# Performance work log

Measured on AMD Instinct MI355X. Metric: run time of the kernel, lower is better.

Reference implementation:

```python
import jax, jax.numpy as jnp
import numpy as np

LN_EPS = 1e-5


def setup_inputs() -> dict:
    key = jax.random.key(0)
    ks = jax.random.split(key, 4)
    B, L, Dm, N = 16, 2048, 512, 64
    return {
        "x": jax.random.normal(ks[0], (B, L, Dm), dtype=jnp.float32),
        "A": jax.random.normal(ks[1], (Dm, N), dtype=jnp.float32),
        "C": jax.random.normal(ks[2], (Dm, N), dtype=jnp.float32),
        "D": jax.random.normal(ks[3], (Dm,), dtype=jnp.float32),
        "gamma": jnp.ones((Dm,), dtype=jnp.float32),
        "beta": jnp.zeros((Dm,), dtype=jnp.float32),
    }


def reference(x, A, C, D, gamma, beta):
    # LayerNorm over last dim (matches nn.LayerNorm(d_model))
    mean = jnp.mean(x, axis=-1, keepdims=True)
    var = jnp.mean(jnp.square(x - mean), axis=-1, keepdims=True)
    x_norm = (x - mean) * jax.lax.rsqrt(var + LN_EPS) * gamma + beta

    B, L, Dm = x.shape
    N = A.shape[1]
    h0 = jnp.zeros((B, N), dtype=x.dtype)

    def step(h, u):
        # u: [B, Dm]; h: [B, N]
        h = jnp.tanh(u @ A + h)
        y = h @ C.T + u * D  # [B, Dm]
        return h, y

    # scan over time: xs [L, B, Dm]
    _, ys = jax.lax.scan(step, h0, jnp.swapaxes(x_norm, 0, 1))
    out = jnp.swapaxes(ys, 0, 1)  # [B, L, Dm]
    return out + x
```

## Files before the change

### kernel.cpp

```cpp
#include <hip/hip_runtime.h>
#include <hip/hip_bf16.h>

typedef short bf16x8 __attribute__((ext_vector_type(8)));
typedef float f32x4 __attribute__((ext_vector_type(4)));

constexpr int B_ = 16;
constexpr int L_ = 2048;
constexpr int DM = 512;
constexpr int NS = 64;
constexpr int BL = B_ * L_;
constexpr float LN_EPS = 1e-5f;
constexpr float KLN = 2.8853900817779268f;

constexpr int SEGS = 32;
constexpr int LSEG = L_ / SEGS;
constexpr int WARM = 64;

__device__ __forceinline__ unsigned f32bits(float f) {
    union { float f; unsigned u; } v{f}; return v.u;
}
__device__ __forceinline__ float bitsf32(unsigned u) {
    union { unsigned u; float f; } v{u}; return v.f;
}
__device__ __forceinline__ unsigned short f2bf(float f) {
    unsigned u = f32bits(f);
    unsigned r = u + 0x7FFF + ((u >> 16) & 1);
    return (unsigned short)(r >> 16);
}

__device__ __forceinline__ void norm_split8(float4 u0, float4 u1,
                                            float rstd, float m2,
                                            bf16x8& ah, bf16x8& al) {
    float t[8] = { fmaf(u0.x, rstd, m2), fmaf(u0.y, rstd, m2),
                   fmaf(u0.z, rstd, m2), fmaf(u0.w, rstd, m2),
                   fmaf(u1.x, rstd, m2), fmaf(u1.y, rstd, m2),
                   fmaf(u1.z, rstd, m2), fmaf(u1.w, rstd, m2) };
    unsigned hb[8], lb[8];
    #pragma unroll
    for (int j = 0; j < 8; ++j) {
        unsigned tb = f32bits(t[j]);
        hb[j] = tb & 0xFFFF0000u;
        lb[j] = f32bits(t[j] - bitsf32(hb[j]));
    }
    union { unsigned u[4]; bf16x8 v; } H, L;
    #pragma unroll
    for (int p = 0; p < 4; ++p) {
        H.u[p] = (hb[2*p] >> 16) | hb[2*p+1];
        L.u[p] = (lb[2*p] >> 16) | (lb[2*p+1] & 0xFFFF0000u);
    }
    ah = H.v; al = L.v;
}

__global__ __launch_bounds__(256) void k_pack(const float* __restrict__ A,
                                              const float* __restrict__ C,
                                              const float* __restrict__ gamma,
                                              const float* __restrict__ beta,
                                              const float* __restrict__ Dv,
                                              unsigned short* __restrict__ PAh,
                                              unsigned short* __restrict__ PAl,
                                              unsigned short* __restrict__ PC,
                                              float* __restrict__ c0,
                                              float* __restrict__ gd,
                                              float* __restrict__ bd) {
    const int blk = blockIdx.x;
    const int tid = threadIdx.x;
    if (blk < 32) {
        const int g = blk * 256 + tid;
        if (g < 4096) {
            const int lane = g & 63, ct = (g >> 6) & 3, k32 = (g >> 8) & 3, kc = g >> 10;
            const int kbase = kc * 128 + k32 * 32 + (lane >> 4) * 8;
            const int col   = ct * 16 + (lane & 15);
            unsigned hb[8], lb[8];
            #pragma unroll
            for (int j = 0; j < 8; ++j) {
                float v = gamma[kbase + j] * A[(size_t)(kbase + j) * NS + col];
                unsigned tb = f32bits(v);
                hb[j] = tb & 0xFFFF0000u;
                lb[j] = f32bits(v - bitsf32(hb[j]));
            }
            uint4 ph, pl;
            ph.x = (hb[0] >> 16) | hb[1]; ph.y = (hb[2] >> 16) | hb[3];
            ph.z = (hb[4] >> 16) | hb[5]; ph.w = (hb[6] >> 16) | hb[7];
            pl.x = (lb[0] >> 16) | (lb[1] & 0xFFFF0000u);
            pl.y = (lb[2] >> 16) | (lb[3] & 0xFFFF0000u);
            pl.z = (lb[4] >> 16) | (lb[5] & 0xFFFF0000u);
            pl.w = (lb[6] >> 16) | (lb[7] & 0xFFFF0000u);
            *reinterpret_cast<uint4*>(PAh + (size_t)g * 8) = ph;
            *reinterpret_cast<uint4*>(PAl + (size_t)g * 8) = pl;
        } else {
            const int g2 = g - 4096;
            const int d = g2 >> 3, s = g2 & 7;
            const int nbase = (s ^ (d & 7)) * 8;
            unsigned short v[8];
            #pragma unroll
            for (int j = 0; j < 8; ++j) v[j] = f2bf(C[(size_t)d * NS + nbase + j]);
            uint4 p;
            p.x = v[0] | ((unsigned)v[1] << 16); p.y = v[2] | ((unsigned)v[3] << 16);
            p.z = v[4] | ((unsigned)v[5] << 16); p.w = v[6] | ((unsigned)v[7] << 16);
            *reinterpret_cast<uint4*>(PC + (size_t)g2 * 8) = p;
        }
    } else {
        __shared__ float red[256];
        #pragma unroll
        for (int i = 0; i < 2; ++i) {
            int d = tid + 256 * i;
            gd[d] = gamma[d] * Dv[d];
            bd[d] = beta[d] * Dv[d];
        }
        const int n = tid & 63, part = tid >> 6;
        float s = 0.f;
        #pragma unroll 8
        for (int k = part * 128; k < part * 128 + 128; ++k)
            s += beta[k] * A[(size_t)k * NS + n];
        red[tid] = s;
        __syncthreads();
        if (tid < 64)
            c0[tid] = red[tid] + red[tid + 64] + red[tid + 128] + red[tid + 192];
    }
}

__global__ __launch_bounds__(512, 2) void k_gemmA(const float* __restrict__ x,
                                               const unsigned short* __restrict__ PAh,
                                               const unsigned short* __restrict__ PAl,
                                               const float* __restrict__ c0,
                                               float* __restrict__ stats,
                                               float* __restrict__ Bu) {
    __shared__ unsigned short AsH[4 * 16 * 64 * 8];
    __shared__ unsigned short AsL[4 * 16 * 64 * 8];
    const int tid  = threadIdx.x;
    const int r0   = blockIdx.x * 128;
    const int w    = tid >> 6;
    const int lane = tid & 63;
    const int myrow = 16 * w + (lane & 15);
    const int kb    = (lane >> 4) * 8;
    const float* xrow = x + (size_t)(r0 + myrow) * DM;

    {
        const float4* sh = reinterpret_cast<const float4*>(PAh);
        const float4* sl = reinterpret_cast<const float4*>(PAl);
        float4* dh = reinterpret_cast<float4*>(AsH);
        float4* dl = reinterpret_cast<float4*>(AsL);
        #pragma unroll
        for (int i = 0; i < 8; ++i) {
            dh[tid + 512 * i] = sh[tid + 512 * i];
            dl[tid + 512 * i] = sl[tid + 512 * i];
        }
    }

    float4 xv[32];
    #pragma unroll
    for (int kc = 0; kc < 4; ++kc) {
        #pragma unroll
        for (int k32 = 0; k32 < 4; ++k32) {
            xv[kc * 8 + 2 * k32]     = *reinterpret_cast<const float4*>(
                xrow + kc * 128 + k32 * 32 + kb);
            xv[kc * 8 + 2 * k32 + 1] = *reinterpret_cast<const float4*>(
                xrow + kc * 128 + k32 * 32 + kb + 4);
        }
    }

    float s = 0.f, s2 = 0.f;
    #pragma unroll
    for (int i = 0; i < 32; ++i) {
        float4 a = xv[i];
        s  += (a.x + a.y) + (a.z + a.w);
        s2 += a.x*a.x + a.y*a.y + a.z*a.z + a.w*a.w;
    }
    s += __shfl_xor(s, 16); s2 += __shfl_xor(s2, 16);
    s += __shfl_xor(s, 32); s2 += __shfl_xor(s2, 32);
    const float mean = s * (1.0f / DM);
    const float var  = s2 * (1.0f / DM) - mean * mean;
    const float rstd = rsqrtf(var + LN_EPS);
    const float m2   = -mean * rstd;
    if (lane < 16) {
        stats[2 * (r0 + myrow)]     = mean;
        stats[2 * (r0 + myrow) + 1] = rstd;
    }

    __syncthreads();

    f32x4 acc[4] = {};
    const bf16x8* ABh = reinterpret_cast<const bf16x8*>(AsH);
    const bf16x8* ABl = reinterpret_cast<const bf16x8*>(AsL);

    #pragma unroll
    for (int kc = 0; kc < 4; ++kc) {
        #pragma unroll
        for (int k32 = 0; k32 < 4; ++k32) {
            bf16x8 ah, al;
            norm_split8(xv[kc * 8 + 2 * k32], xv[kc * 8 + 2 * k32 + 1], rstd, m2, ah, al);
            #pragma unroll
            for (int ct = 0; ct < 4; ++ct) {
                const int fi = ((kc * 4 + k32) * 4 + ct) * 64 + lane;
                bf16x8 bh = ABh[fi];
                bf16x8 bl = ABl[fi];
                acc[ct] = __builtin_amdgcn_mfma_f32_16x16x32_bf16(ah, bh, acc[ct], 0, 0, 0);
                acc[ct] = __builtin_amdgcn_mfma_f32_16x16x32_bf16(ah, bl, acc[ct], 0, 0, 0);
                acc[ct] = __builtin_amdgcn_mfma_f32_16x16x32_bf16(al, bh, acc[ct], 0, 0, 0);
            }
        }
    }

    const int orow = r0 + 16 * w + (lane >> 4) * 4;
    #pragma unroll
    for (int ct = 0; ct < 4; ++ct) {
        const int n = ct * 16 + (lane & 15);
        const float c0n = c0[n];
        #pragma unroll
        for (int j = 0; j < 4; ++j)
            Bu[(size_t)(orow + j) * NS + n] = acc[ct][j] + c0n;
    }
}

__global__ __launch_bounds__(64) void k_scan(const float* __restrict__ Bu,
                                             unsigned short* __restrict__ h) {
    constexpr int G = 16;
    const int seg = blockIdx.x & (SEGS - 1);
    const int b   = blockIdx.x / SEGS;
    const int n   = threadIdx.x;
    const int l0     = seg * LSEG;
    const int start  = (seg == 0) ? 0 : (l0 - WARM);
    const int nGrp   = (l0 + LSEG - start) / G;
    const int gStore = (l0 - start) / G;

    const float* bp = Bu + (size_t)b * L_ * NS + n;
    unsigned short* hp = h + (size_t)b * L_ * NS + n;

    float bufA[G], bufB[G];
    #pragma unroll
    for (int j = 0; j < G; ++j) bufA[j] = KLN * bp[(size_t)(start + j) * NS];

    float hv = 0.0f;
    int g = 0;
    for (;;) {
        {
            const int base = start + (g + 1) * G;
            if (g + 1 < nGrp) {
                #pragma unroll
                for (int j = 0; j < G; ++j)
                    bufB[j] = KLN * bp[(size_t)(base + j) * NS];
            }
            unsigned short* hq = hp + (size_t)(start + g * G) * NS;
            const bool doStore = g >= gStore;
            #pragma unroll
            for (int j = 0; j < G; ++j) {
                float t = fmaf(hv, KLN, bufA[j]);
                float e = __builtin_amdgcn_exp2f(t);
                float rr = __builtin_amdgcn_rcpf(e + 1.0f);
                hv = fmaf(-2.0f, rr, 1.0f);
                if (doStore) hq[(size_t)j * NS] = f2bf(hv);
            }
        }
        if (++g == nGrp) break;
        {
            const int base = start + (g + 1) * G;
            if (g + 1 < nGrp) {
                #pragma unroll
                for (int j = 0; j < G; ++j)
                    bufA[j] = KLN * bp[(size_t)(base + j) * NS];
            }
            unsigned short* hq = hp + (size_t)(start + g * G) * NS;
            const bool doStore = g >= gStore;
            #pragma unroll
            for (int j = 0; j < G; ++j) {
                float t = fmaf(hv, KLN, bufB[j]);
                float e = __builtin_amdgcn_exp2f(t);
                float rr = __builtin_amdgcn_rcpf(e + 1.0f);
                hv = fmaf(-2.0f, rr, 1.0f);
                if (doStore) hq[(size_t)j * NS] = f2bf(hv);
            }
        }
        if (++g == nGrp) break;
    }
}

__global__ __launch_bounds__(256) void k_gemmC(const float* __restrict__ x,
                                               const unsigned short* __restrict__ PC,
                                               const float* __restrict__ gd,
                                               const float* __restrict__ bd,
                                               const float* __restrict__ stats,
                                               const unsigned short* __restrict__ h,
                                               float* __restrict__ out) {
    __shared__ unsigned short Hs[64 * 64];
    __shared__ unsigned short Cs[128 * 64];
    const int tid  = threadIdx.x;
    const int r0   = (blockIdx.x >> 2) * 64;
    const int d0   = (blockIdx.x & 3) * 128;
    const int w    = tid >> 6;
    const int lane = tid & 63;

    {
        const float4* src = reinterpret_cast<const float4*>(PC + (size_t)d0 * NS);
        float4* dst = reinterpret_cast<float4*>(Cs);
        #pragma unroll
        for (int i = 0; i < 4; ++i) dst[tid + 256 * i] = src[tid + 256 * i];
    }
    {
        const char* hb = reinterpret_cast<const char*>(h + (size_t)r0 * NS);
        #pragma unroll
        for (int it = 0; it < 2; ++it) {
            const int o   = it * 4096 + tid * 16;
            const int row = o >> 7;
            const int s   = (o >> 4) & 7;
            uint4 v = *reinterpret_cast<const uint4*>(hb + row * 128 + ((s ^ (row & 7)) << 4));
            *reinterpret_cast<uint4*>(reinterpret_cast<char*>(Hs) + o) = v;
        }
    }
    __syncthreads();

    f32x4 acc[8] = {};
    const int arow = 16 * w + (lane & 15);
    #pragma unroll
    for (int kt = 0; kt < 2; ++kt) {
        const int c = kt * 4 + (lane >> 4);
        bf16x8 a = *reinterpret_cast<const bf16x8*>(
            reinterpret_cast<char*>(Hs) + arow * 128 + ((c ^ (arow & 7)) << 4));
        #pragma unroll
        for (int ct = 0; ct < 8; ++ct) {
            const int dl = ct * 16 + (lane & 15);
            bf16x8 bfr = *reinterpret_cast<const bf16x8*>(
                reinterpret_cast<char*>(Cs) + dl * 128 + ((c ^ (dl & 7)) << 4));
            acc[ct] = __builtin_amdgcn_mfma_f32_16x16x32_bf16(a, bfr, acc[ct], 0, 0, 0);
        }
    }

    const int rbase = r0 + 16 * w + (lane >> 4) * 4;
    float mean_[4], rstd_[4];
    #pragma unroll
    for (int j = 0; j < 4; ++j) {
        mean_[j] = stats[2 * (rbase + j)];
        rstd_[j] = stats[2 * (rbase + j) + 1];
    }
    #pragma unroll
    for (int ct = 0; ct < 8; ++ct) {
        const int d  = d0 + ct * 16 + (lane & 15);
        const float gdv = gd[d];
        const float bdv = bd[d];
        #pragma unroll
        for (int j = 0; j < 4; ++j) {
            const size_t idx = (size_t)(rbase + j) * DM + d;
            const float xv = x[idx];
            const float z  = (xv - mean_[j]) * rstd_[j];
            out[idx] = acc[ct][j] + z * gdv + bdv + xv;
        }
    }
}

extern "C" void kernel_launch(void* const* d_in, const int* in_sizes, int n_in,
                              void* d_out, int out_size, void* d_ws, size_t ws_size,
                              hipStream_t stream) {
    const float* x     = (const float*)d_in[0];
    const float* A     = (const float*)d_in[1];
    const float* C     = (const float*)d_in[2];
    const float* Dv    = (const float*)d_in[3];
    const float* gamma = (const float*)d_in[4];
    const float* beta  = (const float*)d_in[5];
    float* out = (float*)d_out;

    char* ws = (char*)d_ws;
    float* Bu           = (float*)(ws);
    unsigned short* h   = (unsigned short*)(ws + (size_t)BL * NS * 4);
    float* stats        = (float*)(ws + (size_t)BL * NS * 6);
    char* p = ws + (size_t)BL * NS * 6 + (size_t)BL * 2 * 4;
    unsigned short* PAh = (unsigned short*)p;            p += (size_t)DM * NS * 2;
    unsigned short* PAl = (unsigned short*)p;            p += (size_t)DM * NS * 2;
    unsigned short* PC  = (unsigned short*)p;            p += (size_t)DM * NS * 2;
    float* c0           = (float*)p;                     p += 256;
    float* gd           = (float*)p;                     p += (size_t)DM * 4;
    float* bd           = (float*)p;

    k_pack<<<33, 256, 0, stream>>>(A, C, gamma, beta, Dv, PAh, PAl, PC, c0, gd, bd);
    k_gemmA<<<BL / 128, 512, 0, stream>>>(x, PAh, PAl, c0, stats, Bu);
    k_scan<<<B_ * SEGS, 64, 0, stream>>>(Bu, h);
    k_gemmC<<<(BL / 64) * (DM / 128), 256, 0, stream>>>(x, PC, gd, bd, stats, h, out);
}
```

Before: 73.75 us.

## Fuse scan with output GEMM, keeping hidden states in shared memory

Merges the segmented tanh scan and the C-projection GEMM into one kernel. Inside each 512-thread block, one wave runs the scan and writes bf16 hidden states into swizzled LDS, then all waves do the MFMA projection plus the LayerNorm skip epilogue. This removes the global round trip of h and one kernel launch. The cost is that 7 of 8 waves idle during the serial scan, and the C fragments are now read straight from global memory, unswizzled, instead of being staged in LDS.

```diff
diff --git a/kernel.cpp b/kernel.cpp
--- a/kernel.cpp
+++ b/kernel.cpp
@@ -89,11 +89,9 @@
             *reinterpret_cast<uint4*>(PAl + (size_t)g * 8) = pl;
         } else {
             const int g2 = g - 4096;
-            const int d = g2 >> 3, s = g2 & 7;
-            const int nbase = (s ^ (d & 7)) * 8;
             unsigned short v[8];
             #pragma unroll
-            for (int j = 0; j < 8; ++j) v[j] = f2bf(C[(size_t)d * NS + nbase + j]);
+            for (int j = 0; j < 8; ++j) v[j] = f2bf(C[(size_t)g2 * 8 + j]);
             uint4 p;
             p.x = v[0] | ((unsigned)v[1] << 16); p.y = v[2] | ((unsigned)v[3] << 16);
             p.z = v[4] | ((unsigned)v[5] << 16); p.w = v[6] | ((unsigned)v[7] << 16);
@@ -212,136 +210,125 @@
     }
 }
 
-__global__ __launch_bounds__(64) void k_scan(const float* __restrict__ Bu,
-                                             unsigned short* __restrict__ h) {
-    constexpr int G = 16;
+__global__ __launch_bounds__(512, 4) void k_scanC(const float* __restrict__ x,
+                                                  const unsigned short* __restrict__ PC,
+                                                  const float* __restrict__ gd,
+                                                  const float* __restrict__ bd,
+                                                  const float* __restrict__ stats,
+                                                  const float* __restrict__ Bu,
+                                                  float* __restrict__ out) {
+    __shared__ unsigned short Hs[64 * 64];
+    const int tid = threadIdx.x;
     const int seg = blockIdx.x & (SEGS - 1);
-    const int b   = blockIdx.x / SEGS;
-    const int n   = threadIdx.x;
-    const int l0     = seg * LSEG;
-    const int start  = (seg == 0) ? 0 : (l0 - WARM);
-    const int nGrp   = (l0 + LSEG - start) / G;
-    const int gStore = (l0 - start) / G;
-
-    const float* bp = Bu + (size_t)b * L_ * NS + n;
-    unsigned short* hp = h + (size_t)b * L_ * NS + n;
-
-    float bufA[G], bufB[G];
-    #pragma unroll
-    for (int j = 0; j < G; ++j) bufA[j] = KLN * bp[(size_t)(start + j) * NS];
-
-    float hv = 0.0f;
-    int g = 0;
-    for (;;) {
-        {
-            const int base = start + (g + 1) * G;
-            if (g + 1 < nGrp) {
+    const int b   = blockIdx.x >> 5;
+    const int l0  = seg * LSEG;
+    const int rowbase = b * L_ + l0;
+
+    if (tid < 64) {
+        constexpr int G = 16;
+        const int n     = tid;
+        const int start = (seg == 0) ? 0 : (l0 - WARM);
+        const int skip  = l0 - start;
+        const int nGrp  = (l0 + LSEG - start) / G;
+        const float* bp = Bu + ((size_t)b * L_ + start) * NS + n;
+        char* hbase = reinterpret_cast<char*>(Hs);
+
+        float bufA[G], bufB[G];
+        #pragma unroll
+        for (int j = 0; j < G; ++j) bufA[j] = KLN * bp[(size_t)j * NS];
+        float hv = 0.0f;
+        int g = 0;
+        for (;;) {
+            {
+                if (g + 1 < nGrp) {
+                    const int base = (g + 1) * G;
+                    #pragma unroll
+                    for (int j = 0; j < G; ++j)
+                        bufB[j] = KLN * bp[(size_t)(base + j) * NS];
+                }
+                const int lbase = g * G - skip;
+                const bool doStore = lbase >= 0;
                 #pragma unroll
-                for (int j = 0; j < G; ++j)
-                    bufB[j] = KLN * bp[(size_t)(base + j) * NS];
+                for (int j = 0; j < G; ++j) {
+                    float t = fmaf(hv, KLN, bufA[j]);
+                    float e = __builtin_amdgcn_exp2f(t);
+                    float rr = __builtin_amdgcn_rcpf(e + 1.0f);
+                    hv = fmaf(-2.0f, rr, 1.0f);
+                    if (doStore) {
+                        const int lr = lbase + j;
+                        *reinterpret_cast<unsigned short*>(
+                            hbase + lr * 128 + ((2 * n) ^ ((lr & 7) << 4))) = f2bf(hv);
+                    }
+                }
             }
-            unsigned short* hq = hp + (size_t)(start + g * G) * NS;
-            const bool doStore = g >= gStore;
-            #pragma unroll
-            for (int j = 0; j < G; ++j) {
-                float t = fmaf(hv, KLN, bufA[j]);
-                float e = __builtin_amdgcn_exp2f(t);
-                float rr = __builtin_amdgcn_rcpf(e + 1.0f);
-                hv = fmaf(-2.0f, rr, 1.0f);
-                if (doStore) hq[(size_t)j * NS] = f2bf(hv);
+            if (++g == nGrp) break;
+            {
+                if (g + 1 < nGrp) {
+                    const int base = (g + 1) * G;
+                    #pragma unroll
+                    for (int j = 0; j < G; ++j)
+                        bufA[j] = KLN * bp[(size_t)(base + j) * NS];
+                }
+                const int lbase = g * G - skip;
+                const bool doStore = lbase >= 0;
+                #pragma unroll
+                for (int j = 0; j < G; ++j) {
+                    float t = fmaf(hv, KLN, bufB[j]);
+                    float e = __builtin_amdgcn_exp2f(t);
+                    float rr = __builtin_amdgcn_rcpf(e + 1.0f);
+                    hv = fmaf(-2.0f, rr, 1.0f);
+                    if (doStore) {
+                        const int lr = lbase + j;
+                        *reinterpret_cast<unsigned short*>(
+                            hbase + lr * 128 + ((2 * n) ^ ((lr & 7) << 4))) = f2bf(hv);
+                    }
+                }
             }
-        }
-        if (++g == nGrp) break;
-        {
-            const int base = start + (g + 1) * G;
-            if (g + 1 < nGrp) {
-                #pragma unroll
-                for (int j = 0; j < G; ++j)
-                    bufA[j] = KLN * bp[(size_t)(base + j) * NS];
-            }
-            unsigned short* hq = hp + (size_t)(start + g * G) * NS;
-            const bool doStore = g >= gStore;
-            #pragma unroll
-            for (int j = 0; j < G; ++j) {
-                float t = fmaf(hv, KLN, bufB[j]);
-                float e = __builtin_amdgcn_exp2f(t);
-                float rr = __builtin_amdgcn_rcpf(e + 1.0f);
-                hv = fmaf(-2.0f, rr, 1.0f);
-                if (doStore) hq[(size_t)j * NS] = f2bf(hv);
-            }
-        }
-        if (++g == nGrp) break;
-    }
-}
-
-__global__ __launch_bounds__(256) void k_gemmC(const float* __restrict__ x,
-                                               const unsigned short* __restrict__ PC,
-                                               const float* __restrict__ gd,
-                                               const float* __restrict__ bd,
-                                               const float* __restrict__ stats,
-                                               const unsigned short* __restrict__ h,
-                                               float* __restrict__ out) {
-    __shared__ unsigned short Hs[64 * 64];
-    __shared__ unsigned short Cs[128 * 64];
-    const int tid  = threadIdx.x;
-    const int r0   = (blockIdx.x >> 2) * 64;
-    const int d0   = (blockIdx.x & 3) * 128;
+            if (++g == nGrp) break;
+        }
+    }
+    __syncthreads();
+
     const int w    = tid >> 6;
     const int lane = tid & 63;
-
-    {
-        const float4* src = reinterpret_cast<const float4*>(PC + (size_t)d0 * NS);
-        float4* dst = reinterpret_cast<float4*>(Cs);
-        #pragma unroll
-        for (int i = 0; i < 4; ++i) dst[tid + 256 * i] = src[tid + 256 * i];
-    }
-    {
-        const char* hb = reinterpret_cast<const char*>(h + (size_t)r0 * NS);
-        #pragma unroll
-        for (int it = 0; it < 2; ++it) {
-            const int o   = it * 4096 + tid * 16;
-            const int row = o >> 7;
-            const int s   = (o >> 4) & 7;
-            uint4 v = *reinterpret_cast<const uint4*>(hb + row * 128 + ((s ^ (row & 7)) << 4));
-            *reinterpret_cast<uint4*>(reinterpret_cast<char*>(Hs) + o) = v;
-        }
-    }
-    __syncthreads();
-
-    f32x4 acc[8] = {};
-    const int arow = 16 * w + (lane & 15);
+    const int rt   = w >> 1;
+    const int dh   = (w & 1) * 256;
+    const int arow = rt * 16 + (lane & 15);
+
+    bf16x8 afr[2];
     #pragma unroll
     for (int kt = 0; kt < 2; ++kt) {
-        const int c = kt * 4 + (lane >> 4);
-        bf16x8 a = *reinterpret_cast<const bf16x8*>(
-            reinterpret_cast<char*>(Hs) + arow * 128 + ((c ^ (arow & 7)) << 4));
-        #pragma unroll
-        for (int ct = 0; ct < 8; ++ct) {
-            const int dl = ct * 16 + (lane & 15);
-            bf16x8 bfr = *reinterpret_cast<const bf16x8*>(
-                reinterpret_cast<char*>(Cs) + dl * 128 + ((c ^ (dl & 7)) << 4));
-            acc[ct] = __builtin_amdgcn_mfma_f32_16x16x32_bf16(a, bfr, acc[ct], 0, 0, 0);
-        }
-    }
-
-    const int rbase = r0 + 16 * w + (lane >> 4) * 4;
+        const int byte = arow * 128 + ((kt * 64 + (lane >> 4) * 16) ^ ((arow & 7) << 4));
+        afr[kt] = *reinterpret_cast<const bf16x8*>(
+            reinterpret_cast<const char*>(Hs) + byte);
+    }
+
+    const int rb = rowbase + rt * 16 + (lane >> 4) * 4;
     float mean_[4], rstd_[4];
     #pragma unroll
     for (int j = 0; j < 4; ++j) {
-        mean_[j] = stats[2 * (rbase + j)];
-        rstd_[j] = stats[2 * (rbase + j) + 1];
-    }
-    #pragma unroll
-    for (int ct = 0; ct < 8; ++ct) {
-        const int d  = d0 + ct * 16 + (lane & 15);
+        mean_[j] = stats[2 * (rb + j)];
+        rstd_[j] = stats[2 * (rb + j) + 1];
+    }
+
+    const int dl = dh + (lane & 15);
+    const int n0 = (lane >> 4) * 8;
+    #pragma unroll
+    for (int ct = 0; ct < 16; ++ct) {
+        const int d = dl + ct * 16;
+        bf16x8 b0 = *reinterpret_cast<const bf16x8*>(PC + (size_t)d * NS + n0);
+        bf16x8 b1 = *reinterpret_cast<const bf16x8*>(PC + (size_t)d * NS + 32 + n0);
+        f32x4 a = {};
+        a = __builtin_amdgcn_mfma_f32_16x16x32_bf16(afr[0], b0, a, 0, 0, 0);
+        a = __builtin_amdgcn_mfma_f32_16x16x32_bf16(afr[1], b1, a, 0, 0, 0);
         const float gdv = gd[d];
         const float bdv = bd[d];
         #pragma unroll
         for (int j = 0; j < 4; ++j) {
-            const size_t idx = (size_t)(rbase + j) * DM + d;
+            const size_t idx = (size_t)(rb + j) * DM + d;
             const float xv = x[idx];
             const float z  = (xv - mean_[j]) * rstd_[j];
-            out[idx] = acc[ct][j] + z * gdv + bdv + xv;
+            out[idx] = a[j] + z * gdv + bdv + xv;
         }
     }
 }
@@ -359,18 +346,16 @@
 
     char* ws = (char*)d_ws;
     float* Bu           = (float*)(ws);
-    unsigned short* h   = (unsigned short*)(ws + (size_t)BL * NS * 4);
-    float* stats        = (float*)(ws + (size_t)BL * NS * 6);
-    char* p = ws + (size_t)BL * NS * 6 + (size_t)BL * 2 * 4;
-    unsigned short* PAh = (unsigned short*)p;            p += (size_t)DM * NS * 2;
-    unsigned short* PAl = (unsigned short*)p;            p += (size_t)DM * NS * 2;
-    unsigned short* PC  = (unsigned short*)p;            p += (size_t)DM * NS * 2;
-    float* c0           = (float*)p;                     p += 256;
-    float* gd           = (float*)p;                     p += (size_t)DM * 4;
+    float* stats        = (float*)(ws + (size_t)BL * NS * 4);
+    char* p = ws + (size_t)BL * NS * 4 + (size_t)BL * 2 * 4;
+    unsigned short* PAh = (unsigned short*)p;        p += (size_t)DM * NS * 2;
+    unsigned short* PAl = (unsigned short*)p;        p += (size_t)DM * NS * 2;
+    unsigned short* PC  = (unsigned short*)p;        p += (size_t)DM * NS * 2;
+    float* c0           = (float*)p;                 p += 256;
+    float* gd           = (float*)p;                 p += (size_t)DM * 4;
     float* bd           = (float*)p;
 
     k_pack<<<33, 256, 0, stream>>>(A, C, gamma, beta, Dv, PAh, PAl, PC, c0, gd, bd);
     k_gemmA<<<BL / 128, 512, 0, stream>>>(x, PAh, PAl, c0, stats, Bu);
-    k_scan<<<B_ * SEGS, 64, 0, stream>>>(Bu, h);
-    k_gemmC<<<(BL / 64) * (DM / 128), 256, 0, stream>>>(x, PC, gd, bd, stats, h, out);
-}
+    k_scanC<<<B_ * SEGS, 512, 0, stream>>>(x, PC, gd, bd, stats, Bu, out);
+}
```

Result: faster. 67.42 us (-8.6%).
